# Optimization experiments

Measured on AMD Instinct MI355X. Metric: run time of the kernel, lower is better.

Reference implementation:

```python
import jax, jax.numpy as jnp
import numpy as np

B, ACT, DICT = 4096, 768, 12288
TOP_K_AUX = 512
N_DEAD = 1024
AUX_PENALTY = 0.03125
SOFTMAX_AUX_PENALTY = 0.01
L1_COEFF = 0.001  # fraction=1 >= l1_warmup_frac -> full coeff
EPS = 1e-5


def setup_inputs() -> dict:
    key = jax.random.key(0)
    k1, k2, k3 = jax.random.split(key, 3)
    x = jax.random.normal(k1, (B, ACT), dtype=jnp.float32)
    # kaiming-uniform-scale init for W_enc, W_dec = normalized W_enc.T (as in __init__)
    bound = np.sqrt(6.0 / ACT)
    W_enc = jax.random.uniform(k2, (ACT, DICT), dtype=jnp.float32, minval=-bound, maxval=bound)
    W_dec = W_enc.T
    W_dec = W_dec / jnp.linalg.norm(W_dec, axis=-1, keepdims=True)
    b_enc = jnp.zeros((DICT,), dtype=jnp.float32)
    b_dec = jnp.zeros((ACT,), dtype=jnp.float32)
    quantile_threshold = jnp.full((1,), 0.1, dtype=jnp.float32)
    dead_features = jnp.zeros((DICT,), dtype=bool).at[:N_DEAD].set(True)
    return {"x": x, "W_enc": W_enc, "W_dec": W_dec, "b_enc": b_enc,
            "b_dec": b_dec, "quantile_threshold": quantile_threshold,
            "dead_features": dead_features}


def reference(x, W_enc, W_dec, b_enc, b_dec, quantile_threshold, dead_features):
    # input unit-norm (torch .std uses ddof=1)
    x_mean = jnp.mean(x, axis=-1, keepdims=True)
    x = x - x_mean
    x_std = jnp.std(x, axis=-1, keepdims=True, ddof=1)
    x = x / (x_std + EPS)

    x_cent = x - b_dec
    acts_pre = x_cent @ W_enc + b_enc          # [B, DICT]
    acts = jax.nn.relu(acts_pre)

    acts_mask = acts > quantile_threshold
    acts_thresholded = acts * acts_mask
    x_reconstruct = acts_thresholded @ W_dec + b_dec  # [B, ACT]

    residual = x - x_reconstruct

    # aux path 1: topk over dead features only (dead count >= TOP_K_AUX by setup)
    neg_inf = jnp.asarray(-jnp.inf, dtype=acts.dtype)
    masked_acts = jnp.where(dead_features, acts, neg_inf)
    vals, idx = jax.lax.top_k(masked_acts, TOP_K_AUX)  # [B, K]
    rows = jnp.arange(B)[:, None]
    acts_aux = jnp.zeros_like(acts).at[rows, idx].set(vals)  # nonzero only on dead cols
    x_reconstruct_aux = acts_aux @ W_dec + b_dec
    l2_loss_aux = AUX_PENALTY * jnp.mean((x_reconstruct_aux - residual) ** 2)

    # aux path 2: softmax-weighted pre-activations over dead features
    acts_softmax_aux = acts_pre * jax.nn.softmax(acts_pre, axis=-1) * 64.0
    x_reconstruct_softmax = (acts_softmax_aux * dead_features) @ W_dec + b_dec
    l2_loss_softmax = SOFTMAX_AUX_PENALTY * jnp.mean((x_reconstruct_softmax - residual) ** 2)

    l2_loss = jnp.mean((x_reconstruct - x) ** 2)
    l1_norm = jnp.mean(jnp.sum(jnp.abs(acts_thresholded), axis=-1))
    l1_loss = L1_COEFF * l1_norm
    l0_norm = jnp.mean(jnp.sum((acts_thresholded > 0).astype(jnp.float32), axis=-1))

    loss = l2_loss + l1_loss + l2_loss_aux + l2_loss_softmax

    # final rescale (as written in source: * x_std + x, with x the normalized input)
    sae_out = x_reconstruct * x_std + x
    num_dead = jnp.sum(dead_features.astype(jnp.int32))
    return (sae_out, acts_thresholded, loss, l2_loss, l1_loss, l0_norm,
            l1_norm, l2_loss_aux, l2_loss_softmax, num_dead)
```

## Files before the change

kernel.cpp:

```cpp
#include <hip/hip_runtime.h>

#define B_    4096
#define ACT   768
#define DICT  12288
#define KTOP  512
#define NDMAX 1024
#define AUX_PEN  0.03125f
#define SOFT_PEN 0.01f
#define L1_CO    0.001f
#define EPS_     1e-5f
#define NBLK_FE  1536
#define PLANE    (B_ * ACT)
#define SPLITK2  4
#define SPLITK3  2

typedef __attribute__((ext_vector_type(4))) float f32x4;
typedef __attribute__((ext_vector_type(4))) unsigned int u32x4;
typedef __attribute__((ext_vector_type(8))) short short8;
typedef __attribute__((ext_vector_type(8))) __bf16 bf8_t;

__device__ __forceinline__ float b2f(unsigned short u) {
    return __uint_as_float(((unsigned)u) << 16);
}
__device__ __forceinline__ unsigned short f2b(float f) {
    unsigned u = __float_as_uint(f);
    unsigned r = (u + 0x7FFFu + ((u >> 16) & 1u)) >> 16;
    return (unsigned short)r;
}

__device__ __forceinline__ float wredsum(float v) {
#pragma unroll
    for (int o = 32; o; o >>= 1) v += __shfl_down(v, o);
    return v;
}
__device__ __forceinline__ float wredmax(float v) {
#pragma unroll
    for (int o = 32; o; o >>= 1) v = fmaxf(v, __shfl_down(v, o));
    return v;
}
__device__ __forceinline__ int wredsumi(int v) {
#pragma unroll
    for (int o = 32; o; o >>= 1) v += __shfl_down(v, o);
    return v;
}
__device__ __forceinline__ float bredsum(float v, float* sh) {
    int lane = threadIdx.x & 63, w = threadIdx.x >> 6;
    v = wredsum(v);
    __syncthreads();
    if (!lane) sh[w] = v;
    __syncthreads();
    return sh[0] + sh[1] + sh[2] + sh[3];
}
__device__ __forceinline__ float bredmax(float v, float* sh) {
    int lane = threadIdx.x & 63, w = threadIdx.x >> 6;
    v = wredmax(v);
    __syncthreads();
    if (!lane) sh[w] = v;
    __syncthreads();
    return fmaxf(fmaxf(sh[0], sh[1]), fmaxf(sh[2], sh[3]));
}
__device__ __forceinline__ int bredsumi(int v, int* sh) {
    int lane = threadIdx.x & 63, w = threadIdx.x >> 6;
    v = wredsumi(v);
    __syncthreads();
    if (!lane) sh[w] = v;
    __syncthreads();
    return sh[0] + sh[1] + sh[2] + sh[3];
}

__device__ __forceinline__ void gload16(const void* g, const void* lds_base) {
    __builtin_amdgcn_global_load_lds((const __attribute__((address_space(1))) void*)g,
                                     (__attribute__((address_space(3))) void*)lds_base,
                                     16, 0, 0);
}

__global__ __launch_bounds__(256) void norm_kernel(
    const float* __restrict__ x, float* __restrict__ xn,
    unsigned short* __restrict__ xnb, float* __restrict__ xstd)
{
    __shared__ float sh[4];
    const int row = blockIdx.x, t = threadIdx.x;
    const float* xr = x + (size_t)row * ACT;
    float v0 = xr[t], v1 = xr[t + 256], v2 = xr[t + 512];
    float s = bredsum(v0 + v1 + v2, sh);
    float mean = s * (1.0f / ACT);
    v0 -= mean; v1 -= mean; v2 -= mean;
    float s2 = bredsum(v0 * v0 + v1 * v1 + v2 * v2, sh);
    float sd = sqrtf(s2 / (float)(ACT - 1));
    float inv = 1.0f / (sd + EPS_);
    v0 *= inv; v1 *= inv; v2 *= inv;
    size_t base = (size_t)row * ACT;
    xn[base + t] = v0; xn[base + t + 256] = v1; xn[base + t + 512] = v2;
    xnb[base + t] = f2b(v0); xnb[base + t + 256] = f2b(v1); xnb[base + t + 512] = f2b(v2);
    if (!t) xstd[row] = sd;
}

__global__ __launch_bounds__(256) void transpose_bf16(
    const float* __restrict__ in, unsigned short* __restrict__ out, int R, int C)
{
    __shared__ float tile[64][65];
    const int c0 = blockIdx.x * 64, r0 = blockIdx.y * 64;
    const int t = threadIdx.x;
#pragma unroll
    for (int i = 0; i < 16; i++) {
        int lin = t + i * 256;
        int r = lin >> 6, c = lin & 63;
        tile[r][c] = in[(size_t)(r0 + r) * C + c0 + c];
    }
    __syncthreads();
#pragma unroll
    for (int i = 0; i < 16; i++) {
        int lin = t + i * 256;
        int cc = lin >> 6, rr = lin & 63;
        out[(size_t)(c0 + cc) * R + r0 + rr] = f2b(tile[rr][cc]);
    }
}

__global__ __launch_bounds__(256) void cvec_kernel(
    const float* __restrict__ benc, const float* __restrict__ bdec,
    const float* __restrict__ wenc, float* __restrict__ cvec)
{
    int j = blockIdx.x * 256 + threadIdx.x;
    float acc = 0.f;
    for (int k = 0; k < ACT; k++) acc += bdec[k] * wenc[(size_t)k * DICT + j];
    cvec[j] = benc[j] - acc;
}

__global__ __launch_bounds__(256) void dead_scan(
    const void* __restrict__ dead_raw, int* __restrict__ dead_list, int* __restrict__ ndp)
{
    __shared__ int cnt[256];
    const unsigned char* u8 = (const unsigned char*)dead_raw;
    const unsigned* u32p = (const unsigned*)dead_raw;
    unsigned w0 = u32p[0];
    int mode;
    if (w0 == 0x01010101u) mode = 1;
    else if (w0 == 0x3F800000u) mode = 2;
    else if (w0 == 1u) mode = 0;
    else mode = (u8[1] | u8[2] | u8[3]) ? 1 : 0;

    const int t = threadIdx.x;
    const int per = DICT / 256;
    const int base = t * per;
    int c = 0;
    for (int i = 0; i < per; i++) {
        int j = base + i;
        bool d = (mode == 1) ? (u8[j] != 0)
               : (mode == 2) ? (((const float*)dead_raw)[j] != 0.f)
                             : (((const int*)dead_raw)[j] != 0);
        c += d ? 1 : 0;
    }
    cnt[t] = c;
    __syncthreads();
    if (!t) {
        int run = 0;
        for (int i = 0; i < 256; i++) { int v = cnt[i]; cnt[i] = run; run += v; }
        *ndp = run;
    }
    __syncthreads();
    int o = cnt[t];
    for (int i = 0; i < per; i++) {
        int j = base + i;
        bool d = (mode == 1) ? (u8[j] != 0)
               : (mode == 2) ? (((const float*)dead_raw)[j] != 0.f)
                             : (((const int*)dead_raw)[j] != 0);
        if (d) dead_list[o++] = j;
    }
}

__global__ __launch_bounds__(256) void gemm1_kernel(
    const unsigned short* __restrict__ A, const unsigned short* __restrict__ Bt,
    const float* __restrict__ cvec, unsigned short* __restrict__ actspre)
{
    __shared__ __align__(16) unsigned short As[2][128 * 32];
    __shared__ __align__(16) unsigned short Bs[2][128 * 32];
    const int tid = threadIdx.x, lane = tid & 63, wave = tid >> 6;
    const int wr = wave >> 1, wc = wave & 1;
    const int lr = lane & 15, lg = lane >> 4;
    const int flat = blockIdx.x;
    const int xcd = flat & 7, j = flat >> 3;
    const int col0 = (xcd * 12 + (j >> 5)) * 128;
    const int row0 = (j & 31) * 128;
    const int nsteps = ACT / 32;
    f32x4 acc[4][4] = {};

    auto stage = [&](int kt, int b) {
#pragma unroll
        for (int i = 0; i < 2; i++) {
            int c = wave * 2 + i;
            int o = c * 1024;
            int ol = o + lane * 16;
            int r = ol >> 6;
            int cb = (ol & 63) ^ (((r >> 1) & 3) << 4);
            gload16((const char*)A + (size_t)(row0 + r) * (ACT * 2) + kt * 2 + cb,
                    (const char*)As[b] + o);
            gload16((const char*)Bt + (size_t)(col0 + r) * (ACT * 2) + kt * 2 + cb,
                    (const char*)Bs[b] + o);
        }
    };

    stage(0, 0);
    __syncthreads();
    int cur = 0;
    for (int t = 0; t < nsteps; ++t) {
        const int nxt = cur ^ 1;
        if (t + 1 < nsteps) stage((t + 1) * 32, nxt);
        bf8_t af[4], bfr[4];
#pragma unroll
        for (int m = 0; m < 4; m++) {
            int row = wr * 64 + m * 16 + lr;
            af[m] = *(const bf8_t*)((const char*)As[cur] + row * 64 + ((lg * 16) ^ (((row >> 1) & 3) << 4)));
        }
#pragma unroll
        for (int n = 0; n < 4; n++) {
            int col = wc * 64 + n * 16 + lr;
            bfr[n] = *(const bf8_t*)((const char*)Bs[cur] + col * 64 + ((lg * 16) ^ (((col >> 1) & 3) << 4)));
        }
#pragma unroll
        for (int m = 0; m < 4; m++)
#pragma unroll
            for (int n = 0; n < 4; n++)
                acc[m][n] = __builtin_amdgcn_mfma_f32_16x16x32_bf16(af[m], bfr[n], acc[m][n], 0, 0, 0);
        __syncthreads();
        cur = nxt;
    }
#pragma unroll
    for (int m = 0; m < 4; m++) {
        int row = row0 + wr * 64 + m * 16 + lg * 4;
#pragma unroll
        for (int n = 0; n < 4; n++) {
            int col = col0 + wc * 64 + n * 16 + lr;
            float cadd = cvec[col];
#pragma unroll
            for (int r = 0; r < 4; r++) {
                float v = acc[m][n][r] + cadd;
                actspre[(size_t)(row + r) * DICT + col] = f2b(v);
            }
        }
    }
}

__global__ __launch_bounds__(256) void softrow_kernel(
    unsigned short* __restrict__ actspre, const float* __restrict__ qtp,
    const int* __restrict__ dead_list, const int* __restrict__ ndp,
    unsigned short* __restrict__ asoft, unsigned short* __restrict__ aaux,
    float* __restrict__ l1row, float* __restrict__ l0row,
    float* __restrict__ out_thr)
{
    __shared__ __align__(16) unsigned short rowv[DICT];
    __shared__ float shf[4];
    __shared__ int shi[4];
    const int t = threadIdx.x, row = blockIdx.x;
    unsigned short* src = actspre + (size_t)row * DICT;
    float* othr = out_thr + (size_t)row * DICT;
    short8 v[6];
    float mx = -1e30f;
#pragma unroll
    for (int i = 0; i < 6; i++) {
        v[i] = *(const short8*)(src + i * 2048 + t * 8);
        *(short8*)(rowv + i * 2048 + t * 8) = v[i];
#pragma unroll
        for (int e = 0; e < 8; e++) mx = fmaxf(mx, b2f((unsigned short)v[i][e]));
    }
    mx = bredmax(mx, shf);
    const float qt = fmaxf(qtp[0], 0.0f);
    float se = 0.f, l1 = 0.f, l0 = 0.f;
#pragma unroll
    for (int i = 0; i < 6; i++) {
        short8 tvv;
        float tvf[8];
#pragma unroll
        for (int e = 0; e < 8; e++) {
            float f = b2f((unsigned short)v[i][e]);
            se += __expf(f - mx);
            float a = fmaxf(f, 0.f);
            float tv = (a > qt) ? a : 0.f;
            l1 += tv;
            l0 += (tv > 0.f) ? 1.f : 0.f;
            tvv[e] = (tv > 0.f) ? v[i][e] : (short)0;
            tvf[e] = tv;
        }
        *(short8*)(src + i * 2048 + t * 8) = tvv;
        float* od = othr + i * 2048 + t * 8;
        *(f32x4*)od       = (f32x4){ tvf[0], tvf[1], tvf[2], tvf[3] };
        *(f32x4*)(od + 4) = (f32x4){ tvf[4], tvf[5], tvf[6], tvf[7] };
    }
    se = bredsum(se, shf);
    l1 = bredsum(l1, shf);
    l0 = bredsum(l0, shf);
    if (!t) { l1row[row] = l1; l0row[row] = l0; }

    float inv64 = 64.0f / se;
    int nd = *ndp; if (nd > NDMAX) nd = NDMAX;
    unsigned k16[4]; float av_[4];
#pragma unroll
    for (int i = 0; i < 4; i++) {
        int k = t + i * 256;
        float f = 0.f;
        if (k < nd) {
            int idx = dead_list[k];
            f = b2f(rowv[idx]);
            asoft[(size_t)row * NDMAX + k] = f2b(f * __expf(f - mx) * inv64);
        } else {
            asoft[(size_t)row * NDMAX + k] = 0;
        }
        float a = (k < nd) ? fmaxf(f, 0.f) : 0.f;
        av_[i] = a;
        k16[i] = __float_as_uint(a) >> 16;
    }
    unsigned lo = 0u, hi = 0x7F80u;
    while (hi - lo > 1u) {
        unsigned mid = (lo + hi) >> 1;
        int c = 0;
#pragma unroll
        for (int i = 0; i < 4; i++) c += (k16[i] >= mid) ? 1 : 0;
        c = bredsumi(c, shi);
        if (c >= KTOP) lo = mid; else hi = mid;
    }
#pragma unroll
    for (int i = 0; i < 4; i++) {
        int k = t + i * 256;
        aaux[(size_t)row * NDMAX + k] = f2b((k16[i] >= lo) ? av_[i] : 0.f);
    }
}

__global__ __launch_bounds__(256) void wdead_gather(
    const unsigned short* __restrict__ wdec_t, const int* __restrict__ dead_list,
    const int* __restrict__ ndp, unsigned short* __restrict__ wdead)
{
    int n = blockIdx.x;
    int nd = *ndp; if (nd > NDMAX) nd = NDMAX;
    for (int k = threadIdx.x; k < NDMAX; k += 256)
        wdead[(size_t)n * NDMAX + k] = (k < nd) ? wdec_t[(size_t)n * DICT + dead_list[k]] : 0;
}

__global__ __launch_bounds__(256) void gemm2_kernel(
    const unsigned short* __restrict__ Apre, const unsigned short* __restrict__ Bt,
    float* __restrict__ pxrA, float* __restrict__ pxrB)
{
    __shared__ __align__(16) unsigned short As[2][128 * 32];
    __shared__ __align__(16) unsigned short Bs[2][128 * 32];
    const int tid = threadIdx.x, lane = tid & 63, wave = tid >> 6;
    const int wr = wave >> 1, wc = wave & 1;
    const int lr = lane & 15, lg = lane >> 4;
    const int flat = blockIdx.x;
    const int xcd = flat & 7, s = flat >> 3;
    const int q = s / 6, m_ = s - 6 * q;
    const int g = q * 8 + xcd;
    const int col0 = m_ * 128;
    const int row0 = (g & 31) * 128;
    const int zidx = g >> 5;
    const int kbase = zidx * (DICT / SPLITK2);
    const int nsteps = (DICT / SPLITK2) / 32;
    f32x4 acc[4][4] = {};

    auto stage = [&](int kt, int b) {
#pragma unroll
        for (int i = 0; i < 2; i++) {
            int c = wave * 2 + i;
            int o = c * 1024;
            int ol = o + lane * 16;
            int r = ol >> 6;
            int cb = (ol & 63) ^ (((r >> 1) & 3) << 4);
            gload16((const char*)Apre + (size_t)(row0 + r) * (DICT * 2) + (size_t)kt * 2 + cb,
                    (const char*)As[b] + o);
            gload16((const char*)Bt + (size_t)(col0 + r) * (DICT * 2) + (size_t)kt * 2 + cb,
                    (const char*)Bs[b] + o);
        }
    };
    auto compute = [&](int b) {
        bf8_t af[4], bfr[4];
#pragma unroll
        for (int m = 0; m < 4; m++) {
            int row = wr * 64 + m * 16 + lr;
            af[m] = *(const bf8_t*)((const char*)As[b] + row * 64 + ((lg * 16) ^ (((row >> 1) & 3) << 4)));
        }
#pragma unroll
        for (int n = 0; n < 4; n++) {
            int col = wc * 64 + n * 16 + lr;
            bfr[n] = *(const bf8_t*)((const char*)Bs[b] + col * 64 + ((lg * 16) ^ (((col >> 1) & 3) << 4)));
        }
#pragma unroll
        for (int m = 0; m < 4; m++)
#pragma unroll
            for (int n = 0; n < 4; n++)
                acc[m][n] = __builtin_amdgcn_mfma_f32_16x16x32_bf16(af[m], bfr[n], acc[m][n], 0, 0, 0);
    };

    stage(kbase, 0);
    __syncthreads();
    for (int t = 0; t < nsteps; t += 2) {
        stage(kbase + (t + 1) * 32, 1);
        compute(0);
        __syncthreads();
        if (t + 2 < nsteps) stage(kbase + (t + 2) * 32, 0);
        compute(1);
        __syncthreads();
    }
    float* out = (zidx < 2) ? (pxrA + (size_t)zidx * PLANE)
                            : (pxrB + (size_t)(zidx - 2) * PLANE);
#pragma unroll
    for (int m = 0; m < 4; m++) {
        int row = row0 + wr * 64 + m * 16 + lg * 4;
#pragma unroll
        for (int n = 0; n < 4; n++) {
            int col = col0 + wc * 64 + n * 16 + lr;
#pragma unroll
            for (int r = 0; r < 4; r++)
                out[(size_t)(row + r) * ACT + col] = acc[m][n][r];
        }
    }
}

__global__ __launch_bounds__(256) void gemm3_kernel(
    const unsigned short* __restrict__ A1, const unsigned short* __restrict__ A2,
    const unsigned short* __restrict__ Bt,
    float* __restrict__ praux, float* __restrict__ prsoft)
{
    __shared__ __align__(16) unsigned short A1s[128 * 64];
    __shared__ __align__(16) unsigned short A2s[128 * 64];
    __shared__ __align__(16) unsigned short Bs[128 * 64];
    const int tid = threadIdx.x, lane = tid & 63, wave = tid >> 6;
    const int wr = wave >> 1, wc = wave & 1;
    const int lr = lane & 15, lg = lane >> 4;
    const int flat = blockIdx.x;
    const int xcd = flat & 7, s = flat >> 3;
    const int q = s / 6, m_ = s - 6 * q;
    const int g = q * 8 + xcd;
    const int col0 = m_ * 128;
    const int row0 = (g & 31) * 128;
    const int zidx = g >> 5;
    const int kbase = zidx * (NDMAX / SPLITK3);
    const int kend  = kbase + (NDMAX / SPLITK3);
    f32x4 acc1[4][4] = {}, acc2[4][4] = {};

    for (int kt = kbase; kt < kend; kt += 64) {
#pragma unroll
        for (int i = 0; i < 4; i++) {
            int chunk = wave * 4 + i;
            int o = chunk * 1024;
            int ol = o + lane * 16;
            int r = ol >> 7;
            int b = (ol & 127) ^ ((r & 7) << 4);
            gload16((const char*)A1 + (size_t)(row0 + r) * (NDMAX * 2) + kt * 2 + b, (const char*)A1s + o);
            gload16((const char*)A2 + (size_t)(row0 + r) * (NDMAX * 2) + kt * 2 + b, (const char*)A2s + o);
            gload16((const char*)Bt + (size_t)(col0 + r) * (NDMAX * 2) + kt * 2 + b, (const char*)Bs + o);
        }
        __syncthreads();
#pragma unroll
        for (int kk = 0; kk < 64; kk += 32) {
            bf8_t a1f[4], a2f[4], bfr[4];
#pragma unroll
            for (int m = 0; m < 4; m++) {
                int row = wr * 64 + m * 16 + lr;
                int bo = (kk * 2 + lg * 16) ^ ((row & 7) << 4);
                a1f[m] = *(const bf8_t*)((const char*)A1s + row * 128 + bo);
                a2f[m] = *(const bf8_t*)((const char*)A2s + row * 128 + bo);
            }
#pragma unroll
            for (int n = 0; n < 4; n++) {
                int col = wc * 64 + n * 16 + lr;
                bfr[n] = *(const bf8_t*)((const char*)Bs + col * 128 + ((kk * 2 + lg * 16) ^ ((col & 7) << 4)));
            }
#pragma unroll
            for (int m = 0; m < 4; m++)
#pragma unroll
                for (int n = 0; n < 4; n++) {
                    acc1[m][n] = __builtin_amdgcn_mfma_f32_16x16x32_bf16(a1f[m], bfr[n], acc1[m][n], 0, 0, 0);
                    acc2[m][n] = __builtin_amdgcn_mfma_f32_16x16x32_bf16(a2f[m], bfr[n], acc2[m][n], 0, 0, 0);
                }
        }
        __syncthreads();
    }
    float* o1 = praux  + (size_t)zidx * PLANE;
    float* o2 = prsoft + (size_t)zidx * PLANE;
#pragma unroll
    for (int m = 0; m < 4; m++) {
        int row = row0 + wr * 64 + m * 16 + lg * 4;
#pragma unroll
        for (int n = 0; n < 4; n++) {
            int col = col0 + wc * 64 + n * 16 + lr;
#pragma unroll
            for (int r = 0; r < 4; r++) {
                size_t idx = (size_t)(row + r) * ACT + col;
                o1[idx] = acc1[m][n][r];
                o2[idx] = acc2[m][n][r];
            }
        }
    }
}

__global__ __launch_bounds__(256) void final_elem(
    const float* __restrict__ pxrA, const float* __restrict__ pxrB,
    const float* __restrict__ praux, const float* __restrict__ prsoft,
    const float* __restrict__ xn, const float* __restrict__ xstd,
    const float* __restrict__ bdec,
    float* __restrict__ sae_out, float* __restrict__ partials)
{
    __shared__ float sh[4];
    const int t = threadIdx.x, blk = blockIdx.x;
    const int base = blk * 2048;
    float s2 = 0.f, sa = 0.f, ss = 0.f;
#pragma unroll
    for (int i = 0; i < 8; i++) {
        int idx = base + t + i * 256;
        int row = idx / ACT;
        int col = idx - row * ACT;
        float bd = bdec[col];
        float r  = pxrA[idx] + pxrA[PLANE + idx] + pxrB[idx] + pxrB[PLANE + idx] + bd;
        float ra = praux[idx] + praux[PLANE + idx] + bd;
        float rs = prsoft[idx] + prsoft[PLANE + idx] + bd;
        float xv = xn[idx];
        float resid = xv - r;
        float da = ra - resid;
        float dsf = rs - resid;
        s2 += resid * resid;
        sa += da * da;
        ss += dsf * dsf;
        sae_out[idx] = r * xstd[row] + xv;
    }
    s2 = bredsum(s2, sh);
    sa = bredsum(sa, sh);
    ss = bredsum(ss, sh);
    if (!t) {
        partials[blk] = s2;
        partials[NBLK_FE + blk] = sa;
        partials[2 * NBLK_FE + blk] = ss;
    }
}

__global__ __launch_bounds__(256) void final_scalar(
    const float* __restrict__ partials, const float* __restrict__ l1row,
    const float* __restrict__ l0row, const int* __restrict__ ndp,
    float* __restrict__ out_sc)
{
    __shared__ float sh[4];
    const int t = threadIdx.x;
    float s2 = 0.f, sa = 0.f, ss = 0.f;
    for (int i = t; i < NBLK_FE; i += 256) {
        s2 += partials[i];
        sa += partials[NBLK_FE + i];
        ss += partials[2 * NBLK_FE + i];
    }
    s2 = bredsum(s2, sh);
    sa = bredsum(sa, sh);
    ss = bredsum(ss, sh);
    float l1 = 0.f, l0 = 0.f;
    for (int i = t; i < B_; i += 256) { l1 += l1row[i]; l0 += l0row[i]; }
    l1 = bredsum(l1, sh);
    l0 = bredsum(l0, sh);
    if (!t) {
        const float n = (float)B_ * (float)ACT;
        float l2   = s2 / n;
        float l2a  = AUX_PEN  * (sa / n);
        float l2s  = SOFT_PEN * (ss / n);
        float l1n  = l1 / (float)B_;
        float l1l  = L1_CO * l1n;
        float l0n  = l0 / (float)B_;
        float loss = l2 + l1l + l2a + l2s;
        out_sc[0] = loss;
        out_sc[1] = l2;
        out_sc[2] = l1l;
        out_sc[3] = l0n;
        out_sc[4] = l1n;
        out_sc[5] = l2a;
        out_sc[6] = l2s;
        out_sc[7] = (float)(*ndp);
    }
}

extern "C" void kernel_launch(void* const* d_in, const int* in_sizes, int n_in,
                              void* d_out, int out_size, void* d_ws, size_t ws_size,
                              hipStream_t stream)
{
    const float* x    = (const float*)d_in[0];
    const float* Wenc = (const float*)d_in[1];
    const float* Wdec = (const float*)d_in[2];
    const float* benc = (const float*)d_in[3];
    const float* bdec = (const float*)d_in[4];
    const float* qtp  = (const float*)d_in[5];
    const void*  dead = d_in[6];

    float* out_sae = (float*)d_out;
    float* out_thr = out_sae + (size_t)B_ * ACT;
    float* out_sc  = out_thr + (size_t)B_ * DICT;

    char* w = (char*)d_ws;
    auto alloc = [&](size_t bytes) -> char* {
        char* p = w;
        w += (bytes + 255) & ~(size_t)255;
        return p;
    };
    float*          xn      = (float*)alloc((size_t)B_ * ACT * 4);
    unsigned short* xnb     = (unsigned short*)alloc((size_t)B_ * ACT * 2);
    unsigned short* wenc_t  = (unsigned short*)alloc((size_t)DICT * ACT * 2);
    unsigned short* wdec_t  = (unsigned short*)alloc((size_t)ACT * DICT * 2);
    float*          cvec    = (float*)alloc((size_t)DICT * 4);
    unsigned short* actspre = (unsigned short*)alloc((size_t)B_ * DICT * 2);
    unsigned short* asoft   = (unsigned short*)alloc((size_t)B_ * NDMAX * 2);
    unsigned short* aaux    = (unsigned short*)alloc((size_t)B_ * NDMAX * 2);
    unsigned short* wdead   = (unsigned short*)alloc((size_t)ACT * NDMAX * 2);
    float*          xstd    = (float*)alloc((size_t)B_ * 4);
    float*          l1row   = (float*)alloc((size_t)B_ * 4);
    float*          l0row   = (float*)alloc((size_t)B_ * 4);
    float*          partials= (float*)alloc((size_t)3 * NBLK_FE * 4);
    int*            dlist   = (int*)alloc((size_t)DICT * 4);
    int*            ndp     = (int*)alloc(256);
    float*          pxrB    = (float*)alloc((size_t)2 * PLANE * 4);

    float* pxrA = (float*)xnb;
    float* praux  = (float*)actspre;
    float* prsoft = praux + (size_t)SPLITK3 * PLANE;

    norm_kernel<<<B_, 256, 0, stream>>>(x, xn, xnb, xstd);
    transpose_bf16<<<dim3(DICT / 64, ACT / 64), 256, 0, stream>>>(Wenc, wenc_t, ACT, DICT);
    transpose_bf16<<<dim3(ACT / 64, DICT / 64), 256, 0, stream>>>(Wdec, wdec_t, DICT, ACT);
    cvec_kernel<<<DICT / 256, 256, 0, stream>>>(benc, bdec, Wenc, cvec);
    dead_scan<<<1, 256, 0, stream>>>(dead, dlist, ndp);
    gemm1_kernel<<<3072, 256, 0, stream>>>(xnb, wenc_t, cvec, actspre);
    softrow_kernel<<<B_, 256, 0, stream>>>(actspre, qtp, dlist, ndp, asoft, aaux, l1row, l0row, out_thr);
    wdead_gather<<<ACT, 256, 0, stream>>>(wdec_t, dlist, ndp, wdead);
    gemm2_kernel<<<768, 256, 0, stream>>>(actspre, wdec_t, pxrA, pxrB);
    gemm3_kernel<<<384, 256, 0, stream>>>(aaux, asoft, wdead, praux, prsoft);
    final_elem<<<NBLK_FE, 256, 0, stream>>>(pxrA, pxrB, praux, prsoft, xn, xstd, bdec, out_sae, partials);
    final_scalar<<<1, 256, 0, stream>>>(partials, l1row, l0row, ndp, out_sc);
}
```

Baseline: 477.1 us.

## Double-buffer LDS tiles in gemm3 to overlap global loads with MFMA

```diff
diff --git a/kernel.cpp b/kernel.cpp
--- a/kernel.cpp
+++ b/kernel.cpp
@@ -417,9 +417,9 @@
     const unsigned short* __restrict__ Bt,
     float* __restrict__ praux, float* __restrict__ prsoft)
 {
-    __shared__ __align__(16) unsigned short A1s[128 * 64];
-    __shared__ __align__(16) unsigned short A2s[128 * 64];
-    __shared__ __align__(16) unsigned short Bs[128 * 64];
+    __shared__ __align__(16) unsigned short A1s[2][128 * 32];
+    __shared__ __align__(16) unsigned short A2s[2][128 * 32];
+    __shared__ __align__(16) unsigned short Bs[2][128 * 32];
     const int tid = threadIdx.x, lane = tid & 63, wave = tid >> 6;
     const int wr = wave >> 1, wc = wave & 1;
     const int lr = lane & 15, lg = lane >> 4;
@@ -431,45 +431,56 @@
     const int row0 = (g & 31) * 128;
     const int zidx = g >> 5;
     const int kbase = zidx * (NDMAX / SPLITK3);
-    const int kend  = kbase + (NDMAX / SPLITK3);
+    const int nsteps = (NDMAX / SPLITK3) / 32;
     f32x4 acc1[4][4] = {}, acc2[4][4] = {};
 
-    for (int kt = kbase; kt < kend; kt += 64) {
-#pragma unroll
-        for (int i = 0; i < 4; i++) {
-            int chunk = wave * 4 + i;
-            int o = chunk * 1024;
+    auto stage = [&](int kt, int b) {
+#pragma unroll
+        for (int i = 0; i < 2; i++) {
+            int c = wave * 2 + i;
+            int o = c * 1024;
             int ol = o + lane * 16;
-            int r = ol >> 7;
-            int b = (ol & 127) ^ ((r & 7) << 4);
-            gload16((const char*)A1 + (size_t)(row0 + r) * (NDMAX * 2) + kt * 2 + b, (const char*)A1s + o);
-            gload16((const char*)A2 + (size_t)(row0 + r) * (NDMAX * 2) + kt * 2 + b, (const char*)A2s + o);
-            gload16((const char*)Bt + (size_t)(col0 + r) * (NDMAX * 2) + kt * 2 + b, (const char*)Bs + o);
-        }
+            int r = ol >> 6;
+            int cb = (ol & 63) ^ (((r >> 1) & 3) << 4);
+            gload16((const char*)A1 + (size_t)(row0 + r) * (NDMAX * 2) + (size_t)kt * 2 + cb,
+                    (const char*)A1s[b] + o);
+            gload16((const char*)A2 + (size_t)(row0 + r) * (NDMAX * 2) + (size_t)kt * 2 + cb,
+                    (const char*)A2s[b] + o);
+            gload16((const char*)Bt + (size_t)(col0 + r) * (NDMAX * 2) + (size_t)kt * 2 + cb,
+                    (const char*)Bs[b] + o);
+        }
+    };
+    auto compute = [&](int b) {
+        bf8_t a1f[4], a2f[4], bfr[4];
+#pragma unroll
+        for (int m = 0; m < 4; m++) {
+            int row = wr * 64 + m * 16 + lr;
+            int bo = (lg * 16) ^ (((row >> 1) & 3) << 4);
+            a1f[m] = *(const bf8_t*)((const char*)A1s[b] + row * 64 + bo);
+            a2f[m] = *(const bf8_t*)((const char*)A2s[b] + row * 64 + bo);
+        }
+#pragma unroll
+        for (int n = 0; n < 4; n++) {
+            int col = wc * 64 + n * 16 + lr;
+            bfr[n] = *(const bf8_t*)((const char*)Bs[b] + col * 64 + ((lg * 16) ^ (((col >> 1) & 3) << 4)));
+        }
+#pragma unroll
+        for (int m = 0; m < 4; m++)
+#pragma unroll
+            for (int n = 0; n < 4; n++) {
+                acc1[m][n] = __builtin_amdgcn_mfma_f32_16x16x32_bf16(a1f[m], bfr[n], acc1[m][n], 0, 0, 0);
+                acc2[m][n] = __builtin_amdgcn_mfma_f32_16x16x32_bf16(a2f[m], bfr[n], acc2[m][n], 0, 0, 0);
+            }
+    };
+
+    stage(kbase, 0);
+    __syncthreads();
+    for (int t = 0; t < nsteps; t += 2) {
+        stage(kbase + (t + 1) * 32, 1);
+        compute(0);
         __syncthreads();
-#pragma unroll
-        for (int kk = 0; kk < 64; kk += 32) {
-            bf8_t a1f[4], a2f[4], bfr[4];
-#pragma unroll
-            for (int m = 0; m < 4; m++) {
-                int row = wr * 64 + m * 16 + lr;
-                int bo = (kk * 2 + lg * 16) ^ ((row & 7) << 4);
-                a1f[m] = *(const bf8_t*)((const char*)A1s + row * 128 + bo);
-                a2f[m] = *(const bf8_t*)((const char*)A2s + row * 128 + bo);
-            }
-#pragma unroll
-            for (int n = 0; n < 4; n++) {
-                int col = wc * 64 + n * 16 + lr;
-                bfr[n] = *(const bf8_t*)((const char*)Bs + col * 128 + ((kk * 2 + lg * 16) ^ ((col & 7) << 4)));
-            }
-#pragma unroll
-            for (int m = 0; m < 4; m++)
-#pragma unroll
-                for (int n = 0; n < 4; n++) {
-                    acc1[m][n] = __builtin_amdgcn_mfma_f32_16x16x32_bf16(a1f[m], bfr[n], acc1[m][n], 0, 0, 0);
-                    acc2[m][n] = __builtin_amdgcn_mfma_f32_16x16x32_bf16(a2f[m], bfr[n], acc2[m][n], 0, 0, 0);
-                }
-        }
+        if (t + 2 < nsteps) stage(kbase + (t + 2) * 32, 0);
+        compute(1);
         __syncthreads();
     }
     float* o1 = praux  + (size_t)zidx * PLANE;
```

Result: no change. 475.1 us (median of 2 runs) (-0.4%).
